# Optimization experiments

Measured on AMD Instinct MI355X. Metric: run time of the kernel, lower is better.

The kernel has to match this reference:

```python
import jax, jax.numpy as jnp
import numpy as np

N, INC, INN = 8, 32, 50000
OUTC, OUTN, D = 64, 8192, 32  # D = uniform neighbor count (maxD)


def setup_inputs() -> dict:
    key = jax.random.key(0)
    k1, k2, k3, k4, k5 = jax.random.split(key, 5)
    x = jax.random.normal(k1, (N, INC, INN), dtype=jnp.float32)
    nf_weight = jax.random.normal(k2, (INC, INN), dtype=jnp.float32)
    # torch init: uniform(-1,1) * sqrt(6/(1+5*inc)); exact distribution irrelevant for correctness baseline
    ft_weight = (jax.random.uniform(k3, (INC, OUTC), dtype=jnp.float32) * 2.0 - 1.0) * np.sqrt(6.0 / (1.0 + 5 * INC)).astype(np.float32)
    bias = 0.2 * jax.random.normal(k4, (OUTC, OUTN), dtype=jnp.float32)
    A = jax.random.randint(k5, (OUTN, D), 0, INN, dtype=jnp.int32)
    return {"x": x, "nf_weight": nf_weight, "ft_weight": ft_weight, "bias": bias, "A": A}


def reference(x, nf_weight, ft_weight, bias, A):
    # op_order '132': (1) node/feature weight on input, (3) gather+max reduce, (2) feature transform
    y = x * nf_weight                      # (N, inc, inn)
    gathered = y[:, :, A]                  # (N, inc, outn, D) -- padded adjacency gather
    red = jnp.max(gathered, axis=-1)       # (N, inc, outn)    -- reduction='max', mask all-ones (uniform degree)
    out = jnp.einsum('nio,ik->nko', red, ft_weight)  # (N, outc, outn)
    return out + bias                      # bias (outc, outn) broadcast over N
```

## Files before the change

kernel.cpp:

```cpp
#include <hip/hip_runtime.h>
#include <math.h>

#define NN   8
#define INCH 32
#define INN  50000
#define OUTC 64
#define OUTN 8192
#define DD   32
#define CC   256
#define NPL  8
#define PLDW ((size_t)INN * 16)

typedef unsigned short ushortT;

__device__ __forceinline__ unsigned f2bf_u(float f) {
  unsigned u = __float_as_uint(f);
  return (u + 0x7FFFu + ((u >> 16) & 1u)) >> 16;
}


__global__ __launch_bounds__(256) void prep_kernel(
    const float* __restrict__ x, const float* __restrict__ nf, unsigned* __restrict__ yTc) {
  __shared__ ushortT tile[CC][70];
  const int t = threadIdx.x;
  const int j0 = blockIdx.x * 64;
  const int jmax = min(64, INN - j0);
  const int m  = t & 15;
  const int r0 = t >> 4;
  const int lane = t & 63;
  const int wave = t >> 6;

  if (4 * m < jmax) {
    const float4 nv0 = *(const float4*)(nf + (size_t)r0 * INN + j0 + 4 * m);
    const float4 nv1 = *(const float4*)(nf + (size_t)(r0 + 16) * INN + j0 + 4 * m);
    #pragma unroll 8
    for (int p = 0; p < 16; ++p) {
      const int c = (p << 4) + r0;
      const float4 xv = *(const float4*)(x + (size_t)c * INN + j0 + 4 * m);
      const float4 nv = (p & 1) ? nv1 : nv0;
      *(unsigned*)&tile[c][4 * m]     = f2bf_u(xv.x * nv.x) | (f2bf_u(xv.y * nv.y) << 16);
      *(unsigned*)&tile[c][4 * m + 2] = f2bf_u(xv.z * nv.z) | (f2bf_u(xv.w * nv.w) << 16);
    }
  }
  __syncthreads();

  #pragma unroll
  for (int rr = 0; rr < 16; ++rr) {
    const int jl = wave * 16 + rr;
    if (jl < jmax) {
      #pragma unroll
      for (int e = 0; e < 2; ++e) {
        const int clo = lane + 64 * e;
        const unsigned lo = tile[clo][jl];
        const unsigned hi = tile[clo + 128][jl];
        yTc[(size_t)(clo >> 4) * PLDW + (size_t)(j0 + jl) * 16 + (clo & 15)] = lo | (hi << 16);
      }
    }
  }
}

__global__ __launch_bounds__(256, 8) void gather_kernel(
    const unsigned* __restrict__ yTc, const int* __restrict__ A, unsigned* __restrict__ red32) {
  __shared__ int Al[32 * 33];
  const int t = threadIdx.x;
  const int ck = blockIdx.x & 7;
  const int ob = blockIdx.x >> 3;
  const int o0 = ob * 32;

  #pragma unroll
  for (int k = 0; k < 4; ++k) {
    const int f = k * 256 + t;
    Al[(f >> 5) * 33 + (f & 31)] = A[(size_t)o0 * DD + f];
  }
  __syncthreads();

  const unsigned* plane = yTc + (size_t)ck * PLDW;
  const int osub = t >> 3;
  const int cq   = (t >> 1) & 3;
  const int dh   = t & 1;

  float l0 = -INFINITY, l1 = -INFINITY, l2 = -INFINITY, l3 = -INFINITY;
  float h0 = -INFINITY, h1 = -INFINITY, h2 = -INFINITY, h3 = -INFINITY;

  #pragma unroll 8
  for (int k = 0; k < 16; ++k) {
    const int d = 2 * k + dh;
    const int idx = Al[osub * 33 + d];
    const uint4 v = *(const uint4*)(plane + (size_t)idx * 16 + cq * 4);
    l0 = fmaxf(l0, __uint_as_float(v.x << 16));  h0 = fmaxf(h0, __uint_as_float(v.x & 0xffff0000u));
    l1 = fmaxf(l1, __uint_as_float(v.y << 16));  h1 = fmaxf(h1, __uint_as_float(v.y & 0xffff0000u));
    l2 = fmaxf(l2, __uint_as_float(v.z << 16));  h2 = fmaxf(h2, __uint_as_float(v.z & 0xffff0000u));
    l3 = fmaxf(l3, __uint_as_float(v.w << 16));  h3 = fmaxf(h3, __uint_as_float(v.w & 0xffff0000u));
  }
  l0 = fmaxf(l0, __shfl_xor(l0, 1));  h0 = fmaxf(h0, __shfl_xor(h0, 1));
  l1 = fmaxf(l1, __shfl_xor(l1, 1));  h1 = fmaxf(h1, __shfl_xor(h1, 1));
  l2 = fmaxf(l2, __shfl_xor(l2, 1));  h2 = fmaxf(h2, __shfl_xor(h2, 1));
  l3 = fmaxf(l3, __shfl_xor(l3, 1));  h3 = fmaxf(h3, __shfl_xor(h3, 1));

  uint2 pk;
  if (dh == 0) {
    pk.x = (__float_as_uint(l0) >> 16) | (__float_as_uint(h0) & 0xffff0000u);
    pk.y = (__float_as_uint(l1) >> 16) | (__float_as_uint(h1) & 0xffff0000u);
  } else {
    pk.x = (__float_as_uint(l2) >> 16) | (__float_as_uint(h2) & 0xffff0000u);
    pk.y = (__float_as_uint(l3) >> 16) | (__float_as_uint(h3) & 0xffff0000u);
  }
  *(uint2*)(red32 + (size_t)(o0 + osub) * 128 + ck * 16 + cq * 4 + dh * 2) = pk;
}

__global__ __launch_bounds__(256) void out_kernel(
    const unsigned* __restrict__ red32, const float* __restrict__ ft,
    const float* __restrict__ bias, float* __restrict__ out) {
  __shared__ float rtile[64][65];
  __shared__ float ftl[32][64];
  const int t = threadIdx.x;
  const int lane = t & 63;
  const int wave = t >> 6;
  const int np = blockIdx.x >> 7;
  const int ot = blockIdx.x & 127;
  const int o0 = ot * 64;
  const int hi = np >> 1;
  const int sb = (np & 1) * 64;

  #pragma unroll
  for (int q = 0; q < 8; ++q) {
    const int idx = q * 256 + t;
    ftl[idx >> 6][idx & 63] = ft[idx];
  }
  #pragma unroll
  for (int i = 0; i < 2; ++i) {
    const int r = (t >> 3) + 32 * i;
    const int g = t & 7;
    const unsigned* src = red32 + (size_t)(o0 + r) * 128 + sb + g * 8;
    const uint4 v0 = *(const uint4*)(src);
    const uint4 v1 = *(const uint4*)(src + 4);
    const unsigned w[8] = {v0.x, v0.y, v0.z, v0.w, v1.x, v1.y, v1.z, v1.w};
    float* dst = &rtile[r][g * 8];
    #pragma unroll
    for (int u = 0; u < 8; ++u)
      dst[u] = __uint_as_float(hi ? (w[u] & 0xffff0000u) : (w[u] << 16));
  }
  __syncthreads();

  const int n  = np * 2 + (wave & 1);
  const int kh = (wave >> 1) * 32;
  const int cb = (wave & 1) * 32;

  float rv[32];
  #pragma unroll
  for (int i = 0; i < 32; ++i) rv[i] = rtile[lane][cb + i];

  float acc[32];
  #pragma unroll
  for (int kk = 0; kk < 32; ++kk) acc[kk] = 0.f;
  #pragma unroll
  for (int i = 0; i < 32; ++i) {
    #pragma unroll
    for (int kk = 0; kk < 32; ++kk)
      acc[kk] += rv[i] * ftl[i][kh + kk];
  }

  float* op = out + (size_t)n * OUTC * OUTN + o0 + lane;
  const float* bp = bias + o0 + lane;
  #pragma unroll
  for (int kk = 0; kk < 32; ++kk) {
    const int k = kh + kk;
    op[(size_t)k * OUTN] = acc[kk] + bp[(size_t)k * OUTN];
  }
}

extern "C" void kernel_launch(void* const* d_in, const int* in_sizes, int n_in,
                              void* d_out, int out_size, void* d_ws, size_t ws_size,
                              hipStream_t stream) {
  const float* x    = (const float*)d_in[0];
  const float* nf   = (const float*)d_in[1];
  const float* ft   = (const float*)d_in[2];
  const float* bias = (const float*)d_in[3];
  const int*   A    = (const int*)d_in[4];
  float* out = (float*)d_out;

  unsigned* yTc   = (unsigned*)d_ws;
  unsigned* red32 = (unsigned*)((char*)d_ws + NPL * PLDW * 4);

  hipLaunchKernelGGL(prep_kernel,   dim3((INN + 63) / 64),   dim3(256), 0, stream, x, nf, yTc);
  hipLaunchKernelGGL(gather_kernel, dim3((OUTN / 32) * NPL), dim3(256), 0, stream, yTc, A, red32);
  hipLaunchKernelGGL(out_kernel,    dim3(512),               dim3(256), 0, stream, red32, ft, bias, out);
}
```

Before: 46.31 us.

## Restructure prep kernel to emit one contiguous plane chunk per block

The prep kernel now gives each block one of the 8 channel planes and a 512-wide node range, instead of all 256 channels over 64 nodes. The block loads 32 channel rows, multiplies them by the node weights, packs bf16 pairs into a shared-memory tile, and writes one contiguous run of the output plane. The aim is to replace the scattered 4-byte stores across eight planes with fully coalesced contiguous writes. In exchange, the shared-memory tile writes are 2-byte scalar stores that may cause bank conflicts. The weight rows are also loaded again by every plane block rather than reused from registers.

```diff
diff --git a/kernel.cpp b/kernel.cpp
--- a/kernel.cpp
+++ b/kernel.cpp
@@ -10,6 +10,7 @@
 #define CC   256
 #define NPL  8
 #define PLDW ((size_t)INN * 16)
+#define JW   512
 
 typedef unsigned short ushortT;
 
@@ -21,41 +22,40 @@
 
 __global__ __launch_bounds__(256) void prep_kernel(
     const float* __restrict__ x, const float* __restrict__ nf, unsigned* __restrict__ yTc) {
-  __shared__ ushortT tile[CC][70];
+  __shared__ ushortT tile[JW][34];
   const int t = threadIdx.x;
-  const int j0 = blockIdx.x * 64;
-  const int jmax = min(64, INN - j0);
-  const int m  = t & 15;
-  const int r0 = t >> 4;
-  const int lane = t & 63;
-  const int wave = t >> 6;
+  const int p  = blockIdx.x & 7;
+  const int b2 = blockIdx.x >> 3;
+  const int j0 = b2 * JW;
+  const int jmax = min(JW, INN - j0);
 
-  if (4 * m < jmax) {
-    const float4 nv0 = *(const float4*)(nf + (size_t)r0 * INN + j0 + 4 * m);
-    const float4 nv1 = *(const float4*)(nf + (size_t)(r0 + 16) * INN + j0 + 4 * m);
-    #pragma unroll 8
-    for (int p = 0; p < 16; ++p) {
-      const int c = (p << 4) + r0;
-      const float4 xv = *(const float4*)(x + (size_t)c * INN + j0 + 4 * m);
-      const float4 nv = (p & 1) ? nv1 : nv0;
-      *(unsigned*)&tile[c][4 * m]     = f2bf_u(xv.x * nv.x) | (f2bf_u(xv.y * nv.y) << 16);
-      *(unsigned*)&tile[c][4 * m + 2] = f2bf_u(xv.z * nv.z) | (f2bf_u(xv.w * nv.w) << 16);
+  const int rl = t >> 3;
+  const int m  = t & 7;
+  const int cg = p * 16 + (rl & 15) + ((rl >> 4) << 7);
+  const int slot = ((rl & 15) << 1) | (rl >> 4);
+  const float* xr = x + (size_t)cg * INN + j0;
+  const float* nr = nf + (size_t)(((p & 1) << 4) + (rl & 15)) * INN + j0;
+
+  #pragma unroll 8
+  for (int i = 0; i < 16; ++i) {
+    const int jj = i * 32 + m * 4;
+    if (jj < jmax) {
+      const float4 xv = *(const float4*)(xr + jj);
+      const float4 nv = *(const float4*)(nr + jj);
+      tile[jj + 0][slot] = (ushortT)f2bf_u(xv.x * nv.x);
+      tile[jj + 1][slot] = (ushortT)f2bf_u(xv.y * nv.y);
+      tile[jj + 2][slot] = (ushortT)f2bf_u(xv.z * nv.z);
+      tile[jj + 3][slot] = (ushortT)f2bf_u(xv.w * nv.w);
     }
   }
   __syncthreads();
 
-  #pragma unroll
-  for (int rr = 0; rr < 16; ++rr) {
-    const int jl = wave * 16 + rr;
-    if (jl < jmax) {
-      #pragma unroll
-      for (int e = 0; e < 2; ++e) {
-        const int clo = lane + 64 * e;
-        const unsigned lo = tile[clo][jl];
-        const unsigned hi = tile[clo + 128][jl];
-        yTc[(size_t)(clo >> 4) * PLDW + (size_t)(j0 + jl) * 16 + (clo & 15)] = lo | (hi << 16);
-      }
-    }
+  unsigned* dst = yTc + (size_t)p * PLDW + (size_t)j0 * 16;
+  const int ndw = jmax * 16;
+  for (int dw = t; dw < ndw; dw += 256) {
+    const int jl = dw >> 4;
+    const int q  = dw & 15;
+    dst[dw] = *(const unsigned*)&tile[jl][2 * q];
   }
 }
 
@@ -182,7 +182,7 @@
   unsigned* yTc   = (unsigned*)d_ws;
   unsigned* red32 = (unsigned*)((char*)d_ws + NPL * PLDW * 4);
 
-  hipLaunchKernelGGL(prep_kernel,   dim3((INN + 63) / 64),   dim3(256), 0, stream, x, nf, yTc);
-  hipLaunchKernelGGL(gather_kernel, dim3((OUTN / 32) * NPL), dim3(256), 0, stream, yTc, A, red32);
-  hipLaunchKernelGGL(out_kernel,    dim3(512),               dim3(256), 0, stream, red32, ft, bias, out);
+  hipLaunchKernelGGL(prep_kernel,   dim3(((INN + JW - 1) / JW) * NPL), dim3(256), 0, stream, x, nf, yTc);
+  hipLaunchKernelGGL(gather_kernel, dim3((OUTN / 32) * NPL),           dim3(256), 0, stream, yTc, A, red32);
+  hipLaunchKernelGGL(out_kernel,    dim3(512),                         dim3(256), 0, stream, red32, ft, bias, out);
 }
```

Measured after the change: 46.74 us. About the same (+0.9%).
